# Kernel optimization log

Hardware: AMD Instinct MI355X
Metric: run time of the kernel (lower is better)

The kernel has to match this reference:

```python
import jax, jax.numpy as jnp
import numpy as np

IN_F = 2048
OUT_F = 4096
LOW_DIM = 2048
LL_W = OUT_F * IN_F      # 8388608 = 2**23, power of two
LL_B = OUT_F             # 4096 = 2**12


def fwht(v):
    """Fast Walsh-Hadamard transform over a 1-D power-of-two vector (unnormalized),
    matching fast_walsh_hadamard_torched (chunk+cat butterfly)."""
    n = v.shape[0]
    k = int(round(np.log2(n)))
    v = v.reshape((2,) * k)
    for i in range(k):  # loop over log2(n) butterfly stages, not data dims
        a, b = jnp.split(v, 2, axis=i)
        v = jnp.concatenate([a + b, a - b], axis=i)
    return v.reshape(n)


def fastfood(z, dim, BB, GG, Pi):
    """pad -> sign-mul -> WHT -> permute -> Gaussian-mul -> WHT -> slice+scale."""
    LL = BB.shape[0]
    zp = jnp.zeros((LL,), z.dtype).at[: z.shape[0]].set(z)
    m = fwht(BB * zp)
    m = m[Pi] * GG
    m = fwht(m)
    divisor = jnp.sqrt(LL * jnp.sum(GG * GG))
    return m[:dim] / (divisor * np.sqrt(float(dim) / LL))


def setup_inputs() -> dict:
    key = jax.random.key(0)
    ks = jax.random.split(key, 9)
    x = jax.random.normal(ks[0], (4096, IN_F), dtype=jnp.float32)
    low_dim_params = jax.random.normal(ks[1], (LOW_DIM,), dtype=jnp.float32)
    W0 = jax.random.normal(ks[2], (OUT_F, IN_F), dtype=jnp.float32) * 0.02
    b0 = jax.random.normal(ks[3], (OUT_F,), dtype=jnp.float32) * 0.02
    # BB: random +/-1 signs (torch: uniform_(0,2).long()*2-1)
    BB_w = jnp.where(jax.random.uniform(ks[4], (LL_W,)) < 0.5, -1.0, 1.0).astype(jnp.float32)
    GG_w = jax.random.normal(ks[5], (LL_W,), dtype=jnp.float32)
    BB_b = jnp.where(jax.random.uniform(ks[6], (LL_B,)) < 0.5, -1.0, 1.0).astype(jnp.float32)
    GG_b = jax.random.normal(ks[7], (LL_B,), dtype=jnp.float32)
    kp1, kp2 = jax.random.split(ks[8])
    Pi_w = jax.random.permutation(kp1, LL_W).astype(jnp.int64)
    Pi_b = jax.random.permutation(kp2, LL_B).astype(jnp.int64)
    return {"x": x, "low_dim_params": low_dim_params, "W0": W0, "b0": b0,
            "BB_w": BB_w, "GG_w": GG_w, "BB_b": BB_b, "GG_b": GG_b,
            "Pi_w": Pi_w, "Pi_b": Pi_b}


def reference(x, low_dim_params, W0, b0, BB_w, GG_w, BB_b, GG_b, Pi_w, Pi_b):
    # FastfoodWrapper.set_params: param = initial_value + fastfood(low_dim_params)
    dW = fastfood(low_dim_params, OUT_F * IN_F, BB_w, GG_w, Pi_w).reshape(OUT_F, IN_F)
    db = fastfood(low_dim_params, OUT_F, BB_b, GG_b, Pi_b)
    W = W0 + dW
    b = b0 + db
    # base model forward: Linear
    return x @ W.T + b
```

## Files before the change

### kernel.cpp

```cpp
#include <hip/hip_runtime.h>
#include <hip/hip_bf16.h>
#include <math.h>

typedef __bf16  bf16x8 __attribute__((ext_vector_type(8)));
typedef float   f32x4  __attribute__((ext_vector_type(4)));

static __device__ __forceinline__ void load_lds16(const void* g, void* l) {
  __builtin_amdgcn_global_load_lds(
      (const __attribute__((address_space(1))) void*)(g),
      (__attribute__((address_space(3))) void*)(l), 16, 0, 0);
}

#define BAR() asm volatile("s_barrier" ::: "memory")
#define SB0() __builtin_amdgcn_sched_barrier(0)
#define LGKM(N) do { asm volatile("s_waitcnt lgkmcnt(" #N ")" ::: "memory"); SB0(); } while (0)
#define VMC(N) asm volatile("s_waitcnt vmcnt(" #N ")" ::: "memory")

static __device__ __forceinline__ float bf2f(unsigned short u) {
  unsigned int x = ((unsigned int)u) << 16;
  return __builtin_bit_cast(float, x);
}
static __device__ __forceinline__ unsigned short f2bf(float f) {
  __hip_bfloat16 h = __float2bfloat16(f);
  return *reinterpret_cast<unsigned short*>(&h);
}

__global__ __launch_bounds__(256, 4) void k_mid1(
    const float* __restrict__ x, __hip_bfloat16* __restrict__ xb,
    const float* __restrict__ z, const float* __restrict__ BBw,
    const float* __restrict__ b0, const float* __restrict__ BBb,
    const float* __restrict__ GGb, const int* __restrict__ Pib,
    const int* __restrict__ Piw, const float* __restrict__ GGw,
    float* __restrict__ b_buf, float* __restrict__ Sw,
    __hip_bfloat16* __restrict__ m_buf) {
  __shared__ float S[4096];
  __shared__ float red[16];
  const int tid = threadIdx.x;
  const int bid = blockIdx.x;

  if (bid == 1024) {
    for (int i = tid; i < 4096; i += 256)
      S[i] = (i < 2048) ? BBb[i] * z[i] : 0.0f;
    float s = 0.0f;
    for (int i = tid; i < 4096; i += 256) { float g = GGb[i]; s += g * g; }
    for (int off = 32; off > 0; off >>= 1) s += __shfl_down(s, off);
    if ((tid & 63) == 0) red[tid >> 6] = s;
    __syncthreads();
    for (int len = 1; len < 4096; len <<= 1) {
      #pragma unroll
      for (int q = 0; q < 8; ++q) {
        int j = q * 256 + tid;
        int a = ((j & ~(len - 1)) << 1) | (j & (len - 1));
        float xx = S[a], y = S[a + len];
        S[a] = xx + y; S[a + len] = xx - y;
      }
      __syncthreads();
    }
    float v[16];
    #pragma unroll
    for (int q = 0; q < 16; ++q) v[q] = S[Pib[q * 256 + tid]] * GGb[q * 256 + tid];
    __syncthreads();
    #pragma unroll
    for (int q = 0; q < 16; ++q) S[q * 256 + tid] = v[q];
    __syncthreads();
    for (int len = 1; len < 4096; len <<= 1) {
      #pragma unroll
      for (int q = 0; q < 8; ++q) {
        int j = q * 256 + tid;
        int a = ((j & ~(len - 1)) << 1) | (j & (len - 1));
        float xx = S[a], y = S[a + len];
        S[a] = xx + y; S[a + len] = xx - y;
      }
      __syncthreads();
    }
    float Sb = red[0] + red[1] + red[2] + red[3];
    const float scale = 1.0f / sqrtf(Sb * 4096.0f);
    for (int i = tid; i < 4096; i += 256) b_buf[i] = b0[i] + S[i] * scale;
    return;
  }

  const int gtid = bid * 256 + tid;
  #pragma unroll
  for (int i = 0; i < 8; ++i) {
    int q = gtid + i * 262144;
    float4 xv = reinterpret_cast<const float4*>(x)[q];
    ushort4 pk = make_ushort4(f2bf(xv.x), f2bf(xv.y), f2bf(xv.z), f2bf(xv.w));
    reinterpret_cast<ushort4*>(xb)[q] = pk;
  }

  for (int i = tid; i < 2048; i += 256) S[i] = BBw[i] * z[i];
  __syncthreads();
  for (int len = 1; len < 2048; len <<= 1) {
    #pragma unroll
    for (int q = 0; q < 4; ++q) {
      int j = q * 256 + tid;
      int a = ((j & ~(len - 1)) << 1) | (j & (len - 1));
      float xx = S[a], y = S[a + len];
      S[a] = xx + y; S[a + len] = xx - y;
    }
    __syncthreads();
  }

  float ssum = 0.0f;
  const int q6 = tid & 63, w = tid >> 6;
  for (int rr = 0; rr < 4; ++rr) {
    const size_t p0 = ((size_t)bid * 4 + rr) * 2048;
    float v[8];
    #pragma unroll
    for (int h = 0; h < 2; ++h) {
      int4   pv = *reinterpret_cast<const int4*>(&Piw[p0 + tid * 8 + h * 4]);
      float4 gv = *reinterpret_cast<const float4*>(&GGw[p0 + tid * 8 + h * 4]);
      v[h * 4 + 0] = S[pv.x & 2047] * gv.x;
      v[h * 4 + 1] = S[pv.y & 2047] * gv.y;
      v[h * 4 + 2] = S[pv.z & 2047] * gv.z;
      v[h * 4 + 3] = S[pv.w & 2047] * gv.w;
      ssum += gv.x * gv.x + gv.y * gv.y + gv.z * gv.z + gv.w * gv.w;
    }
    #pragma unroll
    for (int st = 0; st < 3; ++st) {
      const int len = 1 << st;
      float t2[8];
      #pragma unroll
      for (int k = 0; k < 8; ++k) {
        int p = k ^ len;
        t2[k] = (k & len) ? v[p] - v[k] : v[k] + v[p];
      }
      #pragma unroll
      for (int k = 0; k < 8; ++k) v[k] = t2[k];
    }
    #pragma unroll
    for (int st = 0; st < 6; ++st) {
      const int xm = 1 << st;
      #pragma unroll
      for (int k = 0; k < 8; ++k) {
        float s2 = __shfl_xor(v[k], xm, 64);
        v[k] = (tid & xm) ? s2 - v[k] : v[k] + s2;
      }
    }
    #pragma unroll
    for (int k = 0; k < 8; ++k) S[2048 + k * 256 + tid] = v[k];
    __syncthreads();
    #pragma unroll
    for (int k = 0; k < 8; ++k) {
      float e0 = S[2048 + k * 256 + q6];
      float e1 = S[2048 + k * 256 + 64 + q6];
      float e2 = S[2048 + k * 256 + 128 + q6];
      float e3 = S[2048 + k * 256 + 192 + q6];
      float t1 = (w & 1) ? e0 - e1 : e0 + e1;
      float t2 = (w & 1) ? e2 - e3 : e2 + e3;
      v[k] = (w & 2) ? t1 - t2 : t1 + t2;
    }
    ushort4 o0 = make_ushort4(f2bf(v[0]), f2bf(v[1]), f2bf(v[2]), f2bf(v[3]));
    ushort4 o1 = make_ushort4(f2bf(v[4]), f2bf(v[5]), f2bf(v[6]), f2bf(v[7]));
    *reinterpret_cast<ushort4*>(&m_buf[p0 + tid * 8])     = o0;
    *reinterpret_cast<ushort4*>(&m_buf[p0 + tid * 8 + 4]) = o1;
    __syncthreads();
  }
  for (int off = 32; off > 0; off >>= 1) ssum += __shfl_down(ssum, off);
  if ((tid & 63) == 0) red[w] = ssum;
  __syncthreads();
  if (tid == 0) atomicAdd(Sw, red[0] + red[1] + red[2] + red[3]);
}

__global__ __launch_bounds__(256, 2) void k_mid2(__hip_bfloat16* __restrict__ m_buf) {
  const int gtid = blockIdx.x * 256 + threadIdx.x;
  const unsigned short* mu = reinterpret_cast<const unsigned short*>(m_buf);
  unsigned short* mw = reinterpret_cast<unsigned short*>(m_buf);
  const int f = gtid & 2047, oh = gtid >> 11;
  const size_t base = (size_t)oh * 131072 + (size_t)f;
  float v[64];
  #pragma unroll
  for (int s = 0; s < 64; ++s) v[s] = bf2f(mu[base + (size_t)s * 2048]);
  #pragma unroll
  for (int len = 1; len < 64; len <<= 1) {
    #pragma unroll
    for (int j = 0; j < 32; ++j) {
      int a = ((j & ~(len - 1)) << 1) | (j & (len - 1));
      float xx = v[a], y = v[a + len];
      v[a] = xx + y; v[a + len] = xx - y;
    }
  }
  #pragma unroll
  for (int s = 0; s < 64; ++s) mw[base + (size_t)s * 2048] = f2bf(v[s]);
}

__global__ __launch_bounds__(256, 2) void k_mid3(const __hip_bfloat16* __restrict__ m_buf,
                                                 const float* __restrict__ W0,
                                                 const float* __restrict__ Sw,
                                                 __hip_bfloat16* __restrict__ Wb) {
  const int gtid = blockIdx.x * 256 + threadIdx.x;
  const unsigned short* mu = reinterpret_cast<const unsigned short*>(m_buf);
  const int f = gtid & 2047, ol = gtid >> 11;
  const size_t base = (size_t)ol * 2048 + (size_t)f;
  float v[64];
  #pragma unroll
  for (int s = 0; s < 64; ++s) v[s] = bf2f(mu[base + (size_t)s * 131072]);
  #pragma unroll
  for (int len = 1; len < 64; len <<= 1) {
    #pragma unroll
    for (int j = 0; j < 32; ++j) {
      int a = ((j & ~(len - 1)) << 1) | (j & (len - 1));
      float xx = v[a], y = v[a + len];
      v[a] = xx + y; v[a + len] = xx - y;
    }
  }
  const float scale = 1.0f / sqrtf((*Sw) * 8388608.0f);
  unsigned short* wbu = reinterpret_cast<unsigned short*>(Wb);
  #pragma unroll
  for (int s = 0; s < 64; ++s) {
    size_t idx = base + (size_t)s * 131072;
    wbu[idx] = f2bf(W0[idx] + v[s] * scale);
  }
}

__global__ __launch_bounds__(512, 2) void k_gemm(const __hip_bfloat16* __restrict__ A,
                                                 const __hip_bfloat16* __restrict__ B,
                                                 const float* __restrict__ bias,
                                                 float* __restrict__ C) {
  constexpr int K = 2048, N = 4096, NT = K / 64;
  __shared__ __hip_bfloat16 As[2][256 * 64];
  __shared__ __hip_bfloat16 Bs[2][256 * 64];
  const int tid = threadIdx.x;
  const int wave = tid >> 6, lane = tid & 63;
  const int bid = blockIdx.x;
  const int swz = (bid & 7) * 32 + (bid >> 3);
  const int row0 = (swz & 15) * 256;
  const int col0 = (swz >> 4) * 256;
  const int wr = wave >> 2, wc = wave & 3;
  const int srow = tid >> 3;
  const int gslot = (tid & 7) ^ (srow & 7);
  const int ldst = tid * 8;
  const int lr = lane & 15, lk = lane >> 4;

  f32x4 acc[8][4] = {};
  bf16x8 a0[4][2], a1[4][2], b0[2][2], b1[2][2];

  #define STAGE_A(BUF, KT, CH0)                                                 \
    { _Pragma("unroll") for (int c = 0; c < 2; ++c)                             \
        load_lds16(A + (size_t)(row0 + (CH0 + c) * 64 + srow) * K + (KT) * 64 + gslot * 8, \
                   &As[BUF][(CH0 + c) * 4096 + ldst]); }
  #define STAGE_B(BUF, KT, CH0)                                                 \
    { _Pragma("unroll") for (int c = 0; c < 2; ++c)                             \
        load_lds16(B + (size_t)(col0 + (CH0 + c) * 64 + srow) * K + (KT) * 64 + gslot * 8, \
                   &Bs[BUF][(CH0 + c) * 4096 + ldst]); }

  #define READ_A(DST, BUF, HALF)                                                \
    { _Pragma("unroll") for (int i = 0; i < 4; ++i)                             \
        _Pragma("unroll") for (int ks = 0; ks < 2; ++ks) {                      \
          int row = wr * 128 + (HALF) * 64 + i * 16 + lr;                       \
          DST[i][ks] = *(const bf16x8*)&As[BUF][row * 64 + (((ks * 4 + lk) ^ (row & 7)) * 8)]; } }
  #define READ_B(DST, BUF, HALF)                                                \
    { _Pragma("unroll") for (int j = 0; j < 2; ++j)                             \
        _Pragma("unroll") for (int ks = 0; ks < 2; ++ks) {                      \
          int row = wc * 64 + (HALF) * 32 + j * 16 + lr;                        \
          DST[j][ks] = *(const bf16x8*)&Bs[BUF][row * 64 + (((ks * 4 + lk) ^ (row & 7)) * 8)]; } }

  #define MFMA16(AF, BF, IO, JO)                                                \
    { __builtin_amdgcn_s_setprio(1);                                            \
      _Pragma("unroll") for (int i = 0; i < 4; ++i)                             \
        _Pragma("unroll") for (int j = 0; j < 2; ++j)                           \
          _Pragma("unroll") for (int ks = 0; ks < 2; ++ks)                      \
            acc[(IO) + i][(JO) + j] =                                           \
              __builtin_amdgcn_mfma_f32_16x16x32_bf16(AF[i][ks], BF[j][ks],     \
                                                      acc[(IO) + i][(JO) + j], 0, 0, 0); \
      __builtin_amdgcn_s_setprio(0); }

  STAGE_A(0, 0, 0) STAGE_B(0, 0, 0) STAGE_A(0, 0, 2) STAGE_B(0, 0, 2)
  STAGE_A(1, 1, 0)
  VMC(2);
  BAR();

  for (int it = 0; it < 16; ++it) {
    const int u = 2 * it;
    const int v = u + 1;
    const int u2 = (u + 2 < NT) ? u + 2 : NT - 1;
    const int u3 = (u + 3 < NT) ? u + 3 : NT - 1;

    READ_A(a0, 0, 0) READ_B(b0, 0, 0)
    STAGE_A(1, v, 2)
    LGKM(8);
    BAR(); LGKM(0);
    MFMA16(a0, b0, 0, 0)
    VMC(4);
    BAR();
    READ_B(b1, 0, 1)
    STAGE_B(1, v, 0)
    BAR(); LGKM(0);
    MFMA16(a0, b1, 0, 2)
    BAR();
    READ_A(a1, 0, 1)
    STAGE_B(1, v, 2)
    BAR(); LGKM(0);
    MFMA16(a1, b1, 4, 2)
    BAR();
    STAGE_A(0, u2, 0)
    BAR();
    MFMA16(a1, b0, 4, 0)
    VMC(4);
    BAR();

    READ_A(a0, 1, 0) READ_B(b0, 1, 0)
    STAGE_B(0, u2, 0)
    LGKM(8);
    BAR(); LGKM(0);
    MFMA16(a0, b0, 0, 0)
    VMC(4);
    BAR();
    READ_B(b1, 1, 1)
    STAGE_A(0, u2, 2)
    BAR(); LGKM(0);
    MFMA16(a0, b1, 0, 2)
    BAR();
    READ_A(a1, 1, 1)
    STAGE_B(0, u2, 2)
    BAR(); LGKM(0);
    MFMA16(a1, b1, 4, 2)
    BAR();
    STAGE_A(1, u3, 0)
    BAR();
    MFMA16(a1, b0, 4, 0)
    VMC(6);
    BAR();
  }

  VMC(0);
  float bv[4];
  #pragma unroll
  for (int j = 0; j < 4; ++j) bv[j] = bias[col0 + wc * 64 + j * 16 + lr];
  float* eps = (float*)&As[0][0];
  #pragma unroll
  for (int r = 0; r < 4; ++r) {
    BAR();
    if (wr == (r >> 1)) {
      const int i0 = (r & 1) * 4;
      #pragma unroll
      for (int i = 0; i < 4; ++i)
        #pragma unroll
        for (int j = 0; j < 4; ++j)
          #pragma unroll
          for (int q = 0; q < 4; ++q) {
            int lrow = i * 16 + lk * 4 + q;
            int col = wc * 64 + j * 16 + lr;
            int sc = ((((col >> 2) ^ (lrow & 7)) << 2) | (col & 3));
            eps[lrow * 256 + sc] = acc[i0 + i][j][q] + bv[j];
          }
    }
    BAR();
    #pragma unroll
    for (int s = 0; s < 8; ++s) {
      int idx = s * 512 + tid;
      int lrow = idx >> 6;
      int g = idx & 63;
      f32x4 vv = *(const f32x4*)&eps[lrow * 256 + ((g ^ (lrow & 7)) << 2)];
      *(f32x4*)&C[(size_t)(row0 + r * 64 + lrow) * N + col0 + g * 4] = vv;
    }
  }
  #undef STAGE_A
  #undef STAGE_B
  #undef READ_A
  #undef READ_B
  #undef MFMA16
}

extern "C" void kernel_launch(void* const* d_in, const int* in_sizes, int n_in,
                              void* d_out, int out_size, void* d_ws, size_t ws_size,
                              hipStream_t stream) {
  (void)in_sizes; (void)n_in; (void)out_size; (void)ws_size;
  const float* x   = (const float*)d_in[0];
  const float* z   = (const float*)d_in[1];
  const float* W0  = (const float*)d_in[2];
  const float* b0  = (const float*)d_in[3];
  const float* BBw = (const float*)d_in[4];
  const float* GGw = (const float*)d_in[5];
  const float* BBb = (const float*)d_in[6];
  const float* GGb = (const float*)d_in[7];
  const int*   Piw = (const int*)d_in[8];
  const int*   Pib = (const int*)d_in[9];
  float* out = (float*)d_out;

  char* ws = (char*)d_ws;
  float*    b_buf = (float*)(ws + 8192);
  float*    Sw    = (float*)(ws + 24576);
  __hip_bfloat16* m_buf = (__hip_bfloat16*)(ws + 32768);
  __hip_bfloat16* Wb = (__hip_bfloat16*)(ws + 32768 + 16777216);
  __hip_bfloat16* xb = (__hip_bfloat16*)(ws + 32768 + 16777216 + 16777216);

  hipMemsetAsync(ws + 24576, 0, 4, stream);
  k_mid1<<<1025, 256, 0, stream>>>(x, xb, z, BBw, b0, BBb, GGb, Pib, Piw, GGw,
                                   b_buf, Sw, m_buf);
  k_mid2<<<512, 256, 0, stream>>>(m_buf);
  k_mid3<<<512, 256, 0, stream>>>(m_buf, W0, Sw, Wb);
  k_gemm<<<256, 512, 0, stream>>>(xb, Wb, b_buf, out);
}
```

Baseline: 146.8 us.

## Widen mid-stage WHT loads to packed bf16 pairs and register-shuffle the 2048-point WHT

k_mid2 and k_mid3 now have each thread process two adjacent columns, loading and storing 32-bit packed bf16 pairs and reading W0 as float2. The grid is halved to 256 blocks to match. This is meant to cut the number of narrow 16-bit memory transactions. The per-block 2048-point WHT in k_mid1 is replaced by an in-register butterfly, wave shuffles and one LDS exchange, instead of 11 LDS passes each followed by a barrier. The trade-off is doubled register arrays (128 floats per thread) in mid2/mid3, which may lower occupancy, and only 256 blocks on the GPU.

```diff
diff --git a/kernel.cpp b/kernel.cpp
--- a/kernel.cpp
+++ b/kernel.cpp
@@ -23,6 +23,9 @@
 static __device__ __forceinline__ unsigned short f2bf(float f) {
   __hip_bfloat16 h = __float2bfloat16(f);
   return *reinterpret_cast<unsigned short*>(&h);
+}
+static __device__ __forceinline__ unsigned pack2bf(float lo, float hi) {
+  return (unsigned)f2bf(lo) | ((unsigned)f2bf(hi) << 16);
 }
 
 __global__ __launch_bounds__(256, 4) void k_mid1(
@@ -80,6 +83,7 @@
   }
 
   const int gtid = bid * 256 + tid;
+  const int q6 = tid & 63, w = tid >> 6;
   #pragma unroll
   for (int i = 0; i < 8; ++i) {
     int q = gtid + i * 262144;
@@ -88,21 +92,59 @@
     reinterpret_cast<ushort4*>(xb)[q] = pk;
   }
 
-  for (int i = tid; i < 2048; i += 256) S[i] = BBw[i] * z[i];
-  __syncthreads();
-  for (int len = 1; len < 2048; len <<= 1) {
-    #pragma unroll
-    for (int q = 0; q < 4; ++q) {
-      int j = q * 256 + tid;
-      int a = ((j & ~(len - 1)) << 1) | (j & (len - 1));
-      float xx = S[a], y = S[a + len];
-      S[a] = xx + y; S[a + len] = xx - y;
-    }
+  {
+    float v[8];
+    float4 b0v = *reinterpret_cast<const float4*>(&BBw[tid * 8]);
+    float4 b1v = *reinterpret_cast<const float4*>(&BBw[tid * 8 + 4]);
+    float4 z0v = *reinterpret_cast<const float4*>(&z[tid * 8]);
+    float4 z1v = *reinterpret_cast<const float4*>(&z[tid * 8 + 4]);
+    v[0] = b0v.x * z0v.x; v[1] = b0v.y * z0v.y;
+    v[2] = b0v.z * z0v.z; v[3] = b0v.w * z0v.w;
+    v[4] = b1v.x * z1v.x; v[5] = b1v.y * z1v.y;
+    v[6] = b1v.z * z1v.z; v[7] = b1v.w * z1v.w;
+    #pragma unroll
+    for (int st = 0; st < 3; ++st) {
+      const int len = 1 << st;
+      float t2[8];
+      #pragma unroll
+      for (int k = 0; k < 8; ++k) {
+        int p = k ^ len;
+        t2[k] = (k & len) ? v[p] - v[k] : v[k] + v[p];
+      }
+      #pragma unroll
+      for (int k = 0; k < 8; ++k) v[k] = t2[k];
+    }
+    #pragma unroll
+    for (int st = 0; st < 6; ++st) {
+      const int xm = 1 << st;
+      #pragma unroll
+      for (int k = 0; k < 8; ++k) {
+        float s2 = __shfl_xor(v[k], xm, 64);
+        v[k] = (tid & xm) ? s2 - v[k] : v[k] + s2;
+      }
+    }
+    #pragma unroll
+    for (int k = 0; k < 8; ++k) S[2048 + k * 256 + tid] = v[k];
+    __syncthreads();
+    #pragma unroll
+    for (int k = 0; k < 8; ++k) {
+      float e0 = S[2048 + k * 256 + q6];
+      float e1 = S[2048 + k * 256 + 64 + q6];
+      float e2 = S[2048 + k * 256 + 128 + q6];
+      float e3 = S[2048 + k * 256 + 192 + q6];
+      float t1 = (w & 1) ? e0 - e1 : e0 + e1;
+      float t2 = (w & 1) ? e2 - e3 : e2 + e3;
+      v[k] = (w & 2) ? t1 - t2 : t1 + t2;
+    }
+    __syncthreads();
+    f32x4 w0 = { v[0], v[1], v[2], v[3] };
+    f32x4 w1 = { v[4], v[5], v[6], v[7] };
+    *reinterpret_cast<f32x4*>(&S[tid * 8])     = w0;
+    *reinterpret_cast<f32x4*>(&S[tid * 8 + 4]) = w1;
     __syncthreads();
   }
 
   float ssum = 0.0f;
-  const int q6 = tid & 63, w = tid >> 6;
   for (int rr = 0; rr < 4; ++rr) {
     const size_t p0 = ((size_t)bid * 4 + rr) * 2048;
     float v[8];
@@ -164,24 +206,30 @@
 
 __global__ __launch_bounds__(256, 2) void k_mid2(__hip_bfloat16* __restrict__ m_buf) {
   const int gtid = blockIdx.x * 256 + threadIdx.x;
-  const unsigned short* mu = reinterpret_cast<const unsigned short*>(m_buf);
-  unsigned short* mw = reinterpret_cast<unsigned short*>(m_buf);
-  const int f = gtid & 2047, oh = gtid >> 11;
-  const size_t base = (size_t)oh * 131072 + (size_t)f;
-  float v[64];
-  #pragma unroll
-  for (int s = 0; s < 64; ++s) v[s] = bf2f(mu[base + (size_t)s * 2048]);
+  const int f2 = gtid & 1023, oh = gtid >> 10;
+  unsigned* mp = reinterpret_cast<unsigned*>(m_buf);
+  const size_t base = (size_t)oh * 65536 + (size_t)f2;
+  float v0[64], v1[64];
+  #pragma unroll
+  for (int s = 0; s < 64; ++s) {
+    unsigned u = mp[base + (size_t)s * 1024];
+    v0[s] = bf2f((unsigned short)(u & 0xffff));
+    v1[s] = bf2f((unsigned short)(u >> 16));
+  }
   #pragma unroll
   for (int len = 1; len < 64; len <<= 1) {
     #pragma unroll
     for (int j = 0; j < 32; ++j) {
       int a = ((j & ~(len - 1)) << 1) | (j & (len - 1));
-      float xx = v[a], y = v[a + len];
-      v[a] = xx + y; v[a + len] = xx - y;
-    }
-  }
-  #pragma unroll
-  for (int s = 0; s < 64; ++s) mw[base + (size_t)s * 2048] = f2bf(v[s]);
+      float xx = v0[a], y = v0[a + len];
+      v0[a] = xx + y; v0[a + len] = xx - y;
+      float xx1 = v1[a], y1 = v1[a + len];
+      v1[a] = xx1 + y1; v1[a + len] = xx1 - y1;
+    }
+  }
+  #pragma unroll
+  for (int s = 0; s < 64; ++s)
+    mp[base + (size_t)s * 1024] = pack2bf(v0[s], v1[s]);
 }
 
 __global__ __launch_bounds__(256, 2) void k_mid3(const __hip_bfloat16* __restrict__ m_buf,
@@ -189,27 +237,34 @@
                                                  const float* __restrict__ Sw,
                                                  __hip_bfloat16* __restrict__ Wb) {
   const int gtid = blockIdx.x * 256 + threadIdx.x;
-  const unsigned short* mu = reinterpret_cast<const unsigned short*>(m_buf);
-  const int f = gtid & 2047, ol = gtid >> 11;
-  const size_t base = (size_t)ol * 2048 + (size_t)f;
-  float v[64];
-  #pragma unroll
-  for (int s = 0; s < 64; ++s) v[s] = bf2f(mu[base + (size_t)s * 131072]);
+  const int f2 = gtid & 1023, ol = gtid >> 10;
+  const unsigned* mp = reinterpret_cast<const unsigned*>(m_buf);
+  const size_t baseu = (size_t)ol * 1024 + (size_t)f2;
+  float v0[64], v1[64];
+  #pragma unroll
+  for (int s = 0; s < 64; ++s) {
+    unsigned u = mp[baseu + (size_t)s * 65536];
+    v0[s] = bf2f((unsigned short)(u & 0xffff));
+    v1[s] = bf2f((unsigned short)(u >> 16));
+  }
   #pragma unroll
   for (int len = 1; len < 64; len <<= 1) {
     #pragma unroll
     for (int j = 0; j < 32; ++j) {
       int a = ((j & ~(len - 1)) << 1) | (j & (len - 1));
-      float xx = v[a], y = v[a + len];
-      v[a] = xx + y; v[a + len] = xx - y;
+      float xx = v0[a], y = v0[a + len];
+      v0[a] = xx + y; v0[a + len] = xx - y;
+      float xx1 = v1[a], y1 = v1[a + len];
+      v1[a] = xx1 + y1; v1[a + len] = xx1 - y1;
     }
   }
   const float scale = 1.0f / sqrtf((*Sw) * 8388608.0f);
-  unsigned short* wbu = reinterpret_cast<unsigned short*>(Wb);
+  unsigned* wbu = reinterpret_cast<unsigned*>(Wb);
   #pragma unroll
   for (int s = 0; s < 64; ++s) {
-    size_t idx = base + (size_t)s * 131072;
-    wbu[idx] = f2bf(W0[idx] + v[s] * scale);
+    size_t eidx = ((size_t)ol * 2048 + (size_t)f2 * 2) + (size_t)s * 131072;
+    float2 wv = *reinterpret_cast<const float2*>(&W0[eidx]);
+    wbu[(eidx >> 1)] = pack2bf(wv.x + v0[s] * scale, wv.y + v1[s] * scale);
   }
 }
 
@@ -388,7 +443,7 @@
   hipMemsetAsync(ws + 24576, 0, 4, stream);
   k_mid1<<<1025, 256, 0, stream>>>(x, xb, z, BBw, b0, BBb, GGb, Pib, Piw, GGw,
                                    b_buf, Sw, m_buf);
-  k_mid2<<<512, 256, 0, stream>>>(m_buf);
-  k_mid3<<<512, 256, 0, stream>>>(m_buf, W0, Sw, Wb);
+  k_mid2<<<256, 256, 0, stream>>>(m_buf);
+  k_mid3<<<256, 256, 0, stream>>>(m_buf, W0, Sw, Wb);
   k_gemm<<<256, 512, 0, stream>>>(xb, Wb, b_buf, out);
 }
```

New measurement: 135.0 us. -8.1%, faster.
